# Performance work log

Hardware: AMD Instinct MI355X
Metric: run time of the kernel (lower is better)

The kernel has to match this reference:

```python
import jax, jax.numpy as jnp
import numpy as np

T, B, I, H = 256, 128, 1024, 1024


def setup_inputs() -> dict:
    key = jax.random.key(0)
    ks = jax.random.split(key, 5)
    # weight init ranges per LSTMLayer.__init__ with wb=0 (no quantization):
    lim_hh = 1.0 / np.sqrt(H)
    lim_ih = 1.0 / np.sqrt(I)
    return {
        "x": jax.random.normal(ks[0], (T, B, I), dtype=jnp.float32),
        "h0": jax.random.normal(ks[1], (B, H), dtype=jnp.float32),
        "c0": jax.random.normal(ks[2], (B, H), dtype=jnp.float32),
        "W_ih": jax.random.uniform(ks[3], (4 * H, I), dtype=jnp.float32, minval=-lim_ih, maxval=lim_ih),
        "W_hh": jax.random.uniform(ks[4], (4 * H, H), dtype=jnp.float32, minval=-lim_hh, maxval=lim_hh),
        "b_ih": jnp.zeros((4 * H,), dtype=jnp.float32),   # uniform_(0, 0)
        "b_hh": jnp.ones((4 * H,), dtype=jnp.float32),    # uniform_(1, 1)
    }


def reference(x, h0, c0, W_ih, W_hh, b_ih, b_hh):
    # Standard LSTM cell, rolled over time with lax.scan.
    # gates layout follows torch LSTMCell: [i, f, g, o] chunks of size H.
    Wih_T = W_ih.T  # [I, 4H]
    Whh_T = W_hh.T  # [H, 4H]
    bias = b_ih + b_hh  # [4H]

    def step(carry, xt):
        h, c = carry  # [B,H] each
        gates = xt @ Wih_T + h @ Whh_T + bias  # [B, 4H]
        i, f, g, o = jnp.split(gates, 4, axis=-1)
        i = jax.nn.sigmoid(i)
        f = jax.nn.sigmoid(f)
        g = jnp.tanh(g)
        o = jax.nn.sigmoid(o)
        c_new = f * c + i * g
        h_new = o * jnp.tanh(c_new)
        return (h_new, c_new), h_new

    (hT, cT), ys = jax.lax.scan(step, (h0, c0), x)
    return ys, hT, cT  # ys: [T, B, H]
```

## Files before the change

### kernel.cpp

```cpp
#include <hip/hip_runtime.h>

#define T_ 256
#define B_ 128
#define I_ 1024
#define H_ 1024
#define G_ 4096
#define BH (B_*H_)
#define TB (T_*B_)

typedef float f32x4 __attribute__((ext_vector_type(4)));
typedef short bf16x8 __attribute__((ext_vector_type(8)));
typedef int   i32x4  __attribute__((ext_vector_type(4)));

__device__ inline unsigned short f2bf(float f) {
    union { float f; unsigned int u; } v; v.f = f;
    unsigned int u = v.u;
    unsigned int r = (u + 0x7fffu + ((u >> 16) & 1u)) >> 16;
    return (unsigned short)r;
}
__device__ inline float bf2f(unsigned short s) {
    union { unsigned int u; float f; } v; v.u = ((unsigned int)s) << 16;
    return v.f;
}
__device__ inline float sigmoidf_(float x) { return 1.0f / (1.0f + __expf(-x)); }
__device__ inline float tanhf_(float x) {
    x = fminf(15.0f, fmaxf(-15.0f, x));
    float e = __expf(2.0f * x);
    return (e - 1.0f) / (e + 1.0f);
}

__device__ __forceinline__ void gload16(const unsigned short* g, unsigned short* l) {
    __builtin_amdgcn_global_load_lds(
        (const __attribute__((address_space(1))) void*)g,
        (__attribute__((address_space(3))) void*)l,
        16, 0, 0);
}

__global__ void cvt_kernel(const float* __restrict__ src, unsigned short* __restrict__ dst, int n) {
    int i = (blockIdx.x * blockDim.x + threadIdx.x) * 4;
    int stride = gridDim.x * blockDim.x * 4;
    for (; i < n; i += stride) {
        float4 v = *reinterpret_cast<const float4*>(src + i);
        ushort4 o;
        o.x = f2bf(v.x); o.y = f2bf(v.y); o.z = f2bf(v.z); o.w = f2bf(v.w);
        *reinterpret_cast<ushort4*>(dst + i) = o;
    }
}

__global__ void cvt_h0_kernel(const float* __restrict__ src, unsigned short* __restrict__ dst, int n) {
    int i = (blockIdx.x * blockDim.x + threadIdx.x) * 4;
    int stride = gridDim.x * blockDim.x * 4;
    for (; i < n; i += stride) {
        float4 v = *reinterpret_cast<const float4*>(src + i);
        ushort4 o;
        o.x = f2bf(v.x) & 0xFFFE; o.y = f2bf(v.y) & 0xFFFE;
        o.z = f2bf(v.z) & 0xFFFE; o.w = f2bf(v.w) & 0xFFFE;
        *reinterpret_cast<ushort4*>(dst + i) = o;
    }
}

__global__ void init_b1_kernel(unsigned* __restrict__ p) {
    int i = (blockIdx.x * blockDim.x + threadIdx.x) * 4;
    i32x4 v = {0x00010001, 0x00010001, 0x00010001, 0x00010001};
    *reinterpret_cast<i32x4*>(p + i) = v;
}

__global__ void bias_kernel(const float* __restrict__ a, const float* __restrict__ b, float* __restrict__ out) {
    int i = blockIdx.x * blockDim.x + threadIdx.x;
    if (i < G_) out[i] = a[i] + b[i];
}

__global__ __launch_bounds__(256, 2) void pregemm(
    const unsigned short* __restrict__ xb,
    const unsigned short* __restrict__ wih,
    const float* __restrict__ bias,
    unsigned short* __restrict__ gx)
{
    __shared__ unsigned short Ab[2][128 * 64];
    __shared__ unsigned short Bb[2][128 * 64];

    int swz = (blockIdx.x & 7) * 1024 + (blockIdx.x >> 3);
    int mg = swz & 255;
    int ng = swz >> 8;
    int m0 = mg * 128, n0 = ng * 128;
    int tid = threadIdx.x;
    int w = tid >> 6, l = tid & 63;
    int qm = (w >> 1) * 64, qn = (w & 1) * 64;
    int lr = l & 15, lkidx = (l >> 4);

    int srow = ((w * 4) * 64 + l) >> 3;
    int sk8  = l & 7;

#define STAGE(BUF, KT)                                                              \
    {                                                                               \
        _Pragma("unroll")                                                           \
        for (int it = 0; it < 4; ++it) {                                            \
            int row = srow + it * 8;                                                \
            gload16(xb  + (size_t)(m0 + row) * I_ + (KT) * 64 + sk8 * 8,            \
                    &Ab[BUF][(w * 4 + it) * 512]);                                  \
            gload16(wih + (size_t)(n0 + row) * I_ + (KT) * 64 + sk8 * 8,            \
                    &Bb[BUF][(w * 4 + it) * 512]);                                  \
        }                                                                           \
    }

    f32x4 acc[4][4] = {};
    int buf = 0;
    STAGE(0, 0)
    __syncthreads();

    for (int kt = 0; kt < 16; ++kt) {
        if (kt + 1 < 16) STAGE(buf ^ 1, kt + 1)
        #pragma unroll
        for (int kk = 0; kk < 2; ++kk) {
            bf16x8 a[4], b[4];
            #pragma unroll
            for (int mt = 0; mt < 4; ++mt)
                a[mt] = *reinterpret_cast<const bf16x8*>(
                    &Ab[buf][(qm + mt * 16 + lr) * 64 + kk * 32 + lkidx * 8]);
            #pragma unroll
            for (int nt = 0; nt < 4; ++nt)
                b[nt] = *reinterpret_cast<const bf16x8*>(
                    &Bb[buf][(qn + nt * 16 + lr) * 64 + kk * 32 + lkidx * 8]);
            #pragma unroll
            for (int mt = 0; mt < 4; ++mt)
                #pragma unroll
                for (int nt = 0; nt < 4; ++nt)
                    acc[mt][nt] = __builtin_amdgcn_mfma_f32_16x16x32_bf16(
                        a[mt], b[nt], acc[mt][nt], 0, 0, 0);
        }
        __syncthreads();
        buf ^= 1;
    }
#undef STAGE

    int lq = l >> 4;
    #pragma unroll
    for (int mt = 0; mt < 4; ++mt) {
        #pragma unroll
        for (int nt = 0; nt < 4; ++nt) {
            #pragma unroll
            for (int r = 0; r < 4; ++r) {
                int m = m0 + qm + mt * 16 + lq * 4 + r;
                int n = n0 + qn + nt * 16 + lr;
                gx[(size_t)m * G_ + n] = f2bf(acc[mt][nt][r] + bias[n]);
            }
        }
    }
}

__global__ __launch_bounds__(512) void lstm_recur(
    const unsigned short* __restrict__ whh,
    const unsigned short* __restrict__ gx,
    const float* __restrict__ c0,
    unsigned short* __restrict__ hbuf,
    float* __restrict__ ys,
    float* __restrict__ hT, float* __restrict__ cT)
{
    __shared__ unsigned short whh_lds[8192 * 8];
    __shared__ float lds_g[4][32][16];

    const int bid = blockIdx.x;
    const int mg  = (bid & 7) >> 1;
    const int ing = (bid >> 3) * 2 + (bid & 1);
    const int m0 = mg * 32, n0 = ing * 16;

    const int tid = threadIdx.x;
    const int w = tid >> 6, l = tid & 63;
    const int mh = w >> 2, kq = w & 3;
    const int lr = l & 15, lkidx = l >> 4;

    for (int it = 0; it < 16; ++it) {
        int idx = it * 512 + tid;
        int row = idx >> 7;
        int ck  = idx & 127;
        int gg = row >> 4, cc = row & 15;
        bf16x8 v = *reinterpret_cast<const bf16x8*>(
            whh + (size_t)(gg * 1024 + n0 + cc) * H_ + ck * 8);
        *reinterpret_cast<bf16x8*>(whh_lds + ((size_t)ck * 64 + row) * 8) = v;
    }
    __syncthreads();

    const unsigned short* bwave = whh_lds + (((size_t)(kq * 32 + lkidx)) * 64 + lr) * 8;

    const int erow = tid >> 4, ecol = tid & 15;
    const size_t eoff = (size_t)(m0 + erow) * H_ + n0 + ecol;
    float c = c0[eoff];
    const unsigned short* gxp = gx + (size_t)(m0 + erow) * G_ + n0 + ecol;

    const size_t hrow = (size_t)(m0 + mh * 16 + lr) * H_ + kq * 256;

    unsigned short gx0 = gxp[0], gx1 = gxp[1024], gx2 = gxp[2048], gx3 = gxp[3072];

    for (int t = 0; t < T_; ++t) {
        const char* hpb = (const char*)hbuf
            + ((size_t)(t & 1) * BH + hrow) * 2 + lkidx * 16;
        const unsigned expw = ((unsigned)((t >> 1) & 1)) * 0x00010001u;
        i32x4 hv0, hv1, hv2, hv3, hv4, hv5, hv6, hv7;
        while (true) {
            asm volatile("global_load_dwordx4 %0, %1, off sc0 sc1"             : "=&v"(hv0) : "v"(hpb));
            asm volatile("global_load_dwordx4 %0, %1, off offset:64 sc0 sc1"   : "=&v"(hv1) : "v"(hpb));
            asm volatile("global_load_dwordx4 %0, %1, off offset:128 sc0 sc1"  : "=&v"(hv2) : "v"(hpb));
            asm volatile("global_load_dwordx4 %0, %1, off offset:192 sc0 sc1"  : "=&v"(hv3) : "v"(hpb));
            asm volatile("global_load_dwordx4 %0, %1, off offset:256 sc0 sc1"  : "=&v"(hv4) : "v"(hpb));
            asm volatile("global_load_dwordx4 %0, %1, off offset:320 sc0 sc1"  : "=&v"(hv5) : "v"(hpb));
            asm volatile("global_load_dwordx4 %0, %1, off offset:384 sc0 sc1"  : "=&v"(hv6) : "v"(hpb));
            asm volatile("global_load_dwordx4 %0, %1, off offset:448 sc0 sc1"  : "=&v"(hv7) : "v"(hpb));
            asm volatile("s_waitcnt vmcnt(0)" ::: "memory");
            __builtin_amdgcn_sched_barrier(0);
            unsigned bad = 0;
#define CHK(HV) bad |= (((unsigned)HV[0] ^ expw) | ((unsigned)HV[1] ^ expw) | \
                        ((unsigned)HV[2] ^ expw) | ((unsigned)HV[3] ^ expw)) & 0x00010001u;
            CHK(hv0) CHK(hv1) CHK(hv2) CHK(hv3) CHK(hv4) CHK(hv5) CHK(hv6) CHK(hv7)
#undef CHK
            if (__all((int)(bad == 0))) break;
            __builtin_amdgcn_s_sleep(4);
        }

        {
            float* lg = (float*)lds_g;
            lg[tid] = 0.f; lg[tid + 512] = 0.f; lg[tid + 1024] = 0.f; lg[tid + 1536] = 0.f;
        }

        f32x4 acc[4] = {};
#define MFMA_K(KK, HV)                                                              \
        {                                                                           \
            bf16x8 av = __builtin_bit_cast(bf16x8, HV);                             \
            _Pragma("unroll")                                                       \
            for (int g4 = 0; g4 < 4; ++g4) {                                        \
                bf16x8 bb = *reinterpret_cast<const bf16x8*>(                       \
                    bwave + (KK) * 2048 + g4 * 128);                                \
                acc[g4] = __builtin_amdgcn_mfma_f32_16x16x32_bf16(                  \
                    av, bb, acc[g4], 0, 0, 0);                                      \
            }                                                                       \
        }
        MFMA_K(0, hv0) MFMA_K(1, hv1) MFMA_K(2, hv2) MFMA_K(3, hv3)
        MFMA_K(4, hv4) MFMA_K(5, hv5) MFMA_K(6, hv6) MFMA_K(7, hv7)
#undef MFMA_K
        __syncthreads();

        #pragma unroll
        for (int g4 = 0; g4 < 4; ++g4)
            #pragma unroll
            for (int r = 0; r < 4; ++r)
                atomicAdd(&lds_g[g4][mh * 16 + lkidx * 4 + r][lr], acc[g4][r]);
        __syncthreads();

        float gi = lds_g[0][erow][ecol] + bf2f(gx0);
        float gf = lds_g[1][erow][ecol] + bf2f(gx1);
        float gg = lds_g[2][erow][ecol] + bf2f(gx2);
        float go = lds_g[3][erow][ecol] + bf2f(gx3);
        float iv = sigmoidf_(gi);
        float fv = sigmoidf_(gf);
        float gv = tanhf_(gg);
        float ov = sigmoidf_(go);
        c = fv * c + iv * gv;
        float hn = ov * tanhf_(c);

        {
            const unsigned wtag = ((unsigned)(t + 1) >> 1) & 1u;
            unsigned us0 = ((unsigned)f2bf(hn) & 0xFFFEu) | wtag;
            float hn_o = __shfl_xor(hn, 1);
            unsigned us1 = ((unsigned)f2bf(hn_o) & 0xFFFEu) | wtag;
            if ((tid & 1) == 0) {
                unsigned u = us0 | (us1 << 16);
                unsigned short* hbn = hbuf + (size_t)((t + 1) & 1) * BH;
                __hip_atomic_store((unsigned*)(hbn + eoff), u,
                                   __ATOMIC_RELAXED, __HIP_MEMORY_SCOPE_AGENT);
            }
        }
        ys[(size_t)t * BH + eoff] = hn;
        if (t == T_ - 1) { hT[eoff] = hn; cT[eoff] = c; }

        if (t + 1 < T_) {
            const unsigned short* p = gxp + (size_t)(t + 1) * B_ * G_;
            gx0 = p[0]; gx1 = p[1024]; gx2 = p[2048]; gx3 = p[3072];
        }

        __syncthreads();
    }
}

extern "C" void kernel_launch(void* const* d_in, const int* in_sizes, int n_in,
                              void* d_out, int out_size, void* d_ws, size_t ws_size,
                              hipStream_t stream)
{
    const float* x   = (const float*)d_in[0];
    const float* h0  = (const float*)d_in[1];
    const float* c0  = (const float*)d_in[2];
    const float* Wih = (const float*)d_in[3];
    const float* Whh = (const float*)d_in[4];
    const float* bih = (const float*)d_in[5];
    const float* bhh = (const float*)d_in[6];

    char* ws = (char*)d_ws;
    unsigned short* gx   = (unsigned short*)(ws);
    unsigned short* xb   = (unsigned short*)(ws + 268435456);
    unsigned short* wihb = (unsigned short*)(ws + 335544320);
    unsigned short* whhb = (unsigned short*)(ws + 343932928);
    unsigned short* hbuf = (unsigned short*)(ws + 352321536);
    float*          bias = (float*)(ws + 352845824);

    float* out = (float*)d_out;
    float* ys = out;
    float* hT = out + (size_t)TB * H_;
    float* cT = hT + BH;

    cvt_kernel<<<2048, 256, 0, stream>>>(x,   xb,   TB * I_);
    cvt_kernel<<<512,  256, 0, stream>>>(Wih, wihb, G_ * I_);
    cvt_kernel<<<512,  256, 0, stream>>>(Whh, whhb, G_ * H_);
    cvt_h0_kernel<<<128, 256, 0, stream>>>(h0, hbuf, BH);
    init_b1_kernel<<<64, 256, 0, stream>>>((unsigned*)(hbuf + BH));
    bias_kernel<<<16, 256, 0, stream>>>(bih, bhh, bias);

    pregemm<<<8192, 256, 0, stream>>>(xb, wihb, bias, gx);

    lstm_recur<<<256, 512, 0, stream>>>(whhb, gx, c0, hbuf, ys, hT, cT);
}
```

Baseline: 4.172 ms.

## Fuse input projection GEMM into recurrent kernel, overlapping with h-dependency wait

```diff
diff --git a/kernel.cpp b/kernel.cpp
--- a/kernel.cpp
+++ b/kernel.cpp
@@ -27,13 +27,6 @@
     x = fminf(15.0f, fmaxf(-15.0f, x));
     float e = __expf(2.0f * x);
     return (e - 1.0f) / (e + 1.0f);
-}
-
-__device__ __forceinline__ void gload16(const unsigned short* g, unsigned short* l) {
-    __builtin_amdgcn_global_load_lds(
-        (const __attribute__((address_space(1))) void*)g,
-        (__attribute__((address_space(3))) void*)l,
-        16, 0, 0);
 }
 
 __global__ void cvt_kernel(const float* __restrict__ src, unsigned short* __restrict__ dst, int n) {
@@ -70,87 +63,11 @@
     if (i < G_) out[i] = a[i] + b[i];
 }
 
-__global__ __launch_bounds__(256, 2) void pregemm(
-    const unsigned short* __restrict__ xb,
-    const unsigned short* __restrict__ wih,
-    const float* __restrict__ bias,
-    unsigned short* __restrict__ gx)
-{
-    __shared__ unsigned short Ab[2][128 * 64];
-    __shared__ unsigned short Bb[2][128 * 64];
-
-    int swz = (blockIdx.x & 7) * 1024 + (blockIdx.x >> 3);
-    int mg = swz & 255;
-    int ng = swz >> 8;
-    int m0 = mg * 128, n0 = ng * 128;
-    int tid = threadIdx.x;
-    int w = tid >> 6, l = tid & 63;
-    int qm = (w >> 1) * 64, qn = (w & 1) * 64;
-    int lr = l & 15, lkidx = (l >> 4);
-
-    int srow = ((w * 4) * 64 + l) >> 3;
-    int sk8  = l & 7;
-
-#define STAGE(BUF, KT)                                                              \
-    {                                                                               \
-        _Pragma("unroll")                                                           \
-        for (int it = 0; it < 4; ++it) {                                            \
-            int row = srow + it * 8;                                                \
-            gload16(xb  + (size_t)(m0 + row) * I_ + (KT) * 64 + sk8 * 8,            \
-                    &Ab[BUF][(w * 4 + it) * 512]);                                  \
-            gload16(wih + (size_t)(n0 + row) * I_ + (KT) * 64 + sk8 * 8,            \
-                    &Bb[BUF][(w * 4 + it) * 512]);                                  \
-        }                                                                           \
-    }
-
-    f32x4 acc[4][4] = {};
-    int buf = 0;
-    STAGE(0, 0)
-    __syncthreads();
-
-    for (int kt = 0; kt < 16; ++kt) {
-        if (kt + 1 < 16) STAGE(buf ^ 1, kt + 1)
-        #pragma unroll
-        for (int kk = 0; kk < 2; ++kk) {
-            bf16x8 a[4], b[4];
-            #pragma unroll
-            for (int mt = 0; mt < 4; ++mt)
-                a[mt] = *reinterpret_cast<const bf16x8*>(
-                    &Ab[buf][(qm + mt * 16 + lr) * 64 + kk * 32 + lkidx * 8]);
-            #pragma unroll
-            for (int nt = 0; nt < 4; ++nt)
-                b[nt] = *reinterpret_cast<const bf16x8*>(
-                    &Bb[buf][(qn + nt * 16 + lr) * 64 + kk * 32 + lkidx * 8]);
-            #pragma unroll
-            for (int mt = 0; mt < 4; ++mt)
-                #pragma unroll
-                for (int nt = 0; nt < 4; ++nt)
-                    acc[mt][nt] = __builtin_amdgcn_mfma_f32_16x16x32_bf16(
-                        a[mt], b[nt], acc[mt][nt], 0, 0, 0);
-        }
-        __syncthreads();
-        buf ^= 1;
-    }
-#undef STAGE
-
-    int lq = l >> 4;
-    #pragma unroll
-    for (int mt = 0; mt < 4; ++mt) {
-        #pragma unroll
-        for (int nt = 0; nt < 4; ++nt) {
-            #pragma unroll
-            for (int r = 0; r < 4; ++r) {
-                int m = m0 + qm + mt * 16 + lq * 4 + r;
-                int n = n0 + qn + nt * 16 + lr;
-                gx[(size_t)m * G_ + n] = f2bf(acc[mt][nt][r] + bias[n]);
-            }
-        }
-    }
-}
-
 __global__ __launch_bounds__(512) void lstm_recur(
     const unsigned short* __restrict__ whh,
-    const unsigned short* __restrict__ gx,
+    const unsigned short* __restrict__ wih,
+    const unsigned short* __restrict__ xb,
+    const float* __restrict__ bias,
     const float* __restrict__ c0,
     unsigned short* __restrict__ hbuf,
     float* __restrict__ ys,
@@ -158,6 +75,7 @@
 {
     __shared__ unsigned short whh_lds[8192 * 8];
     __shared__ float lds_g[4][32][16];
+    __shared__ float lds_gx[4][32][16];
 
     const int bid = blockIdx.x;
     const int mg  = (bid & 7) >> 1;
@@ -178,6 +96,10 @@
             whh + (size_t)(gg * 1024 + n0 + cc) * H_ + ck * 8);
         *reinterpret_cast<bf16x8*>(whh_lds + ((size_t)ck * 64 + row) * 8) = v;
     }
+    {
+        float* lgx = (float*)lds_gx;
+        lgx[tid] = 0.f; lgx[tid + 512] = 0.f; lgx[tid + 1024] = 0.f; lgx[tid + 1536] = 0.f;
+    }
     __syncthreads();
 
     const unsigned short* bwave = whh_lds + (((size_t)(kq * 32 + lkidx)) * 64 + lr) * 8;
@@ -185,13 +107,57 @@
     const int erow = tid >> 4, ecol = tid & 15;
     const size_t eoff = (size_t)(m0 + erow) * H_ + n0 + ecol;
     float c = c0[eoff];
-    const unsigned short* gxp = gx + (size_t)(m0 + erow) * G_ + n0 + ecol;
+    const float bias_i = bias[n0 + ecol];
+    const float bias_f = bias[1024 + n0 + ecol];
+    const float bias_g = bias[2048 + n0 + ecol];
+    const float bias_o = bias[3072 + n0 + ecol];
 
     const size_t hrow = (size_t)(m0 + mh * 16 + lr) * H_ + kq * 256;
-
-    unsigned short gx0 = gxp[0], gx1 = gxp[1024], gx2 = gxp[2048], gx3 = gxp[3072];
+    const unsigned short* wihb_g = wih + (size_t)(n0 + lr) * I_ + kq * 256 + lkidx * 8;
+
+    bf16x8 ax[8];
+    f32x4 accx[4];
+
+#define XLOAD(TT)                                                                   \
+    {                                                                               \
+        const unsigned short* xp = xb                                               \
+            + (size_t)((TT) * B_ + m0 + mh * 16 + lr) * I_ + kq * 256 + lkidx * 8;  \
+        _Pragma("unroll")                                                           \
+        for (int kk = 0; kk < 8; ++kk)                                              \
+            ax[kk] = *reinterpret_cast<const bf16x8*>(xp + kk * 32);                \
+    }
+#define XGEMM()                                                                     \
+    {                                                                               \
+        _Pragma("unroll")                                                           \
+        for (int g4 = 0; g4 < 4; ++g4) {                                            \
+            const unsigned short* wp = wihb_g + (size_t)g4 * 1024 * I_;             \
+            bf16x8 bw[8];                                                           \
+            _Pragma("unroll")                                                       \
+            for (int kk = 0; kk < 8; ++kk)                                          \
+                bw[kk] = *reinterpret_cast<const bf16x8*>(wp + kk * 32);            \
+            accx[g4] = (f32x4){0.f, 0.f, 0.f, 0.f};                                 \
+            _Pragma("unroll")                                                       \
+            for (int kk = 0; kk < 8; ++kk)                                          \
+                accx[g4] = __builtin_amdgcn_mfma_f32_16x16x32_bf16(                 \
+                    ax[kk], bw[kk], accx[g4], 0, 0, 0);                             \
+        }                                                                           \
+    }
+#define XADD()                                                                      \
+    {                                                                               \
+        _Pragma("unroll")                                                           \
+        for (int g4 = 0; g4 < 4; ++g4)                                              \
+            _Pragma("unroll")                                                       \
+            for (int r = 0; r < 4; ++r)                                             \
+                atomicAdd(&lds_gx[g4][mh * 16 + lkidx * 4 + r][lr], accx[g4][r]);   \
+    }
+
+    XLOAD(0)
+    XGEMM()
+    XADD()
 
     for (int t = 0; t < T_; ++t) {
+        if (t + 1 < T_) XLOAD(t + 1)
+
         const char* hpb = (const char*)hbuf
             + ((size_t)(t & 1) * BH + hrow) * 2 + lkidx * 16;
         const unsigned expw = ((unsigned)((t >> 1) & 1)) * 0x00010001u;
@@ -213,7 +179,7 @@
             CHK(hv0) CHK(hv1) CHK(hv2) CHK(hv3) CHK(hv4) CHK(hv5) CHK(hv6) CHK(hv7)
 #undef CHK
             if (__all((int)(bad == 0))) break;
-            __builtin_amdgcn_s_sleep(4);
+            __builtin_amdgcn_s_sleep(2);
         }
 
         {
@@ -243,12 +209,15 @@
             #pragma unroll
             for (int r = 0; r < 4; ++r)
                 atomicAdd(&lds_g[g4][mh * 16 + lkidx * 4 + r][lr], acc[g4][r]);
-        __syncthreads();
-
-        float gi = lds_g[0][erow][ecol] + bf2f(gx0);
-        float gf = lds_g[1][erow][ecol] + bf2f(gx1);
-        float gg = lds_g[2][erow][ecol] + bf2f(gx2);
-        float go = lds_g[3][erow][ecol] + bf2f(gx3);
+
+        if (t + 1 < T_) XGEMM()
+
+        __syncthreads();
+
+        float gi = lds_g[0][erow][ecol] + lds_gx[0][erow][ecol] + bias_i;
+        float gf = lds_g[1][erow][ecol] + lds_gx[1][erow][ecol] + bias_f;
+        float gg = lds_g[2][erow][ecol] + lds_gx[2][erow][ecol] + bias_g;
+        float go = lds_g[3][erow][ecol] + lds_gx[3][erow][ecol] + bias_o;
         float iv = sigmoidf_(gi);
         float fv = sigmoidf_(gf);
         float gv = tanhf_(gg);
@@ -271,13 +240,19 @@
         ys[(size_t)t * BH + eoff] = hn;
         if (t == T_ - 1) { hT[eoff] = hn; cT[eoff] = c; }
 
+        __syncthreads();
+
         if (t + 1 < T_) {
-            const unsigned short* p = gxp + (size_t)(t + 1) * B_ * G_;
-            gx0 = p[0]; gx1 = p[1024]; gx2 = p[2048]; gx3 = p[3072];
-        }
-
-        __syncthreads();
-    }
+            float* lgx = (float*)lds_gx;
+            lgx[tid] = 0.f; lgx[tid + 512] = 0.f; lgx[tid + 1024] = 0.f; lgx[tid + 1536] = 0.f;
+        }
+        __syncthreads();
+
+        if (t + 1 < T_) XADD()
+    }
+#undef XLOAD
+#undef XGEMM
+#undef XADD
 }
 
 extern "C" void kernel_launch(void* const* d_in, const int* in_sizes, int n_in,
@@ -293,12 +268,11 @@
     const float* bhh = (const float*)d_in[6];
 
     char* ws = (char*)d_ws;
-    unsigned short* gx   = (unsigned short*)(ws);
-    unsigned short* xb   = (unsigned short*)(ws + 268435456);
-    unsigned short* wihb = (unsigned short*)(ws + 335544320);
-    unsigned short* whhb = (unsigned short*)(ws + 343932928);
-    unsigned short* hbuf = (unsigned short*)(ws + 352321536);
-    float*          bias = (float*)(ws + 352845824);
+    unsigned short* xb   = (unsigned short*)(ws);
+    unsigned short* wihb = (unsigned short*)(ws + 67108864);
+    unsigned short* whhb = (unsigned short*)(ws + 75497472);
+    unsigned short* hbuf = (unsigned short*)(ws + 83886080);
+    float*          bias = (float*)(ws + 84410368);
 
     float* out = (float*)d_out;
     float* ys = out;
@@ -312,7 +286,5 @@
     init_b1_kernel<<<64, 256, 0, stream>>>((unsigned*)(hbuf + BH));
     bias_kernel<<<16, 256, 0, stream>>>(bih, bhh, bias);
 
-    pregemm<<<8192, 256, 0, stream>>>(xb, wihb, bias, gx);
-
-    lstm_recur<<<256, 512, 0, stream>>>(whhb, gx, c0, hbuf, ys, hT, cT);
-}
+    lstm_recur<<<256, 512, 0, stream>>>(whhb, wihb, xb, bias, c0, hbuf, ys, hT, cT);
+}
```

New measurement: 6.471 ms. +55.1%, slower.
